# Kernel optimization log

Measured on AMD Instinct MI355X. Metric: run time of the kernel, lower is better.

Reference implementation:

```python
import jax, jax.numpy as jnp
import numpy as np

T = 4096        # sequence length
D = 128         # input feature dim
TRACE = 64      # trace_size
CONTEXT = 64    # context_size
HID = 64        # internal dense width (hardcoded 64 in module)
OUT = 128       # output_size
LN_EPS = 1e-6   # flax LayerNorm default epsilon


def setup_inputs() -> dict:
    key = jax.random.key(0)
    ks = jax.random.split(key, 12)

    def dense(k, fi, fo):
        return (jax.random.normal(k, (fi, fo), jnp.float32) / np.sqrt(fi).astype(np.float32))

    inp = {}
    inp["x"] = jax.random.normal(ks[0], (T, D), jnp.float32)
    inp["state"] = jnp.zeros((1, TRACE, CONTEXT), jnp.complex64)
    inp["start"] = jax.random.uniform(ks[1], (T,)) < 0.01  # sparse episode resets
    # deterministic FFM decay / frequency params (init_deterministic)
    inp["a"] = jnp.linspace(1e-6, 0.5, TRACE).astype(jnp.float32)
    inp["b"] = (2.0 * jnp.pi / jnp.linspace(1.0, 1000.0, CONTEXT)).astype(jnp.float32)
    inp["W1"] = dense(ks[2], D, HID);               inp["b1"] = jnp.zeros((HID,), jnp.float32)
    inp["W2"] = dense(ks[3], HID, 2 * TRACE);       inp["b2"] = jnp.zeros((2 * TRACE,), jnp.float32)
    inp["Wgi"] = dense(ks[4], 2 * TRACE, TRACE);    inp["bgi"] = jnp.zeros((TRACE,), jnp.float32)
    inp["Wp"] = dense(ks[5], 2 * TRACE, TRACE);     inp["bp"] = jnp.zeros((TRACE,), jnp.float32)
    inp["Wz"] = dense(ks[6], 2 * TRACE * CONTEXT, HID); inp["bz"] = jnp.zeros((HID,), jnp.float32)
    inp["Wgo"] = dense(ks[7], 2 * TRACE, HID);      inp["bgo"] = jnp.zeros((HID,), jnp.float32)
    inp["Ws"] = dense(ks[8], 2 * TRACE, HID);       inp["bs"] = jnp.zeros((HID,), jnp.float32)
    inp["W3"] = dense(ks[9], HID, HID);             inp["b3"] = jnp.zeros((HID,), jnp.float32)
    inp["W4"] = dense(ks[10], HID, OUT);            inp["b4"] = jnp.zeros((OUT,), jnp.float32)
    return inp


def _ffm_scan(scan_in, state0, start, a, b):
    # scan_in: (T, TRACE, CONTEXT) float, state0: (1, TRACE, CONTEXT) complex64
    t = scan_in.shape[0]
    timestep = jnp.ones((t + 1, 1, 1), dtype=jnp.int32)
    start_f = jnp.concatenate(
        [jnp.zeros((1, 1, 1), dtype=bool), start.reshape(t, 1, 1)], axis=0)
    xs = jnp.concatenate([state0, scan_in.astype(jnp.complex64)], axis=0)

    neg_a = -jnp.abs(a).reshape(1, TRACE, 1)
    b_r = b.reshape(1, 1, CONTEXT)
    ab = neg_a + 1j * b_r  # (1, TRACE, CONTEXT) complex

    def gamma(j):
        # j: (N,1,1) int -> (N, TRACE, CONTEXT) complex decay
        return jnp.exp(ab * j.astype(jnp.float32))

    def combine(carry, incoming):
        prev_start, s, i = carry
        st, xx, j = incoming
        keep = jnp.logical_not(st)
        s = s * keep
        j = j * keep.astype(j.dtype)
        new_s = s * gamma(j) + xx
        return (jnp.logical_or(st, prev_start), new_s, j + i)

    _, new_state, _ = jax.lax.associative_scan(
        combine, (start_f, xs, timestep), axis=0)
    return new_state[1:]  # (T, TRACE, CONTEXT) complex64


def _layernorm(x):
    mu = jnp.mean(x, axis=-1, keepdims=True)
    var = jnp.var(x, axis=-1, keepdims=True)
    return (x - mu) * jax.lax.rsqrt(var + LN_EPS)


def _forward(x, state, start, a, b, W1, b1, W2, b2, Wgi, bgi, Wp, bp,
             Wz, bz, Wgo, bgo, Ws, bs, W3, b3, W4, b4):
    h = jax.nn.relu(x @ W1 + b1)                 # (T, 64)
    h2 = h @ W2 + b2                             # (T, 2*TRACE)
    gate_in = jax.nn.sigmoid(h2 @ Wgi + bgi)     # (T, TRACE)
    pre = jax.nn.sigmoid(h2 @ Wp + bp)           # (T, TRACE)
    gated = pre * gate_in                        # (T, TRACE)
    scan_in = jnp.broadcast_to(gated[:, :, None], (gated.shape[0], TRACE, CONTEXT))
    state_seq = _ffm_scan(scan_in, state, start, a, b)  # (T, TRACE, CONTEXT) c64
    z_in = jnp.concatenate([jnp.real(state_seq), jnp.imag(state_seq)],
                           axis=-1).reshape(state_seq.shape[0], -1)
    z = z_in @ Wz + bz                           # (T, 64)
    gate_out = jax.nn.sigmoid(h2 @ Wgo + bgo)    # (T, 64)
    skip = h2 @ Ws + bs                          # (T, 64)
    out = _layernorm(z * gate_out) + skip * (1.0 - gate_out)
    out = jax.nn.relu(out @ W3 + b3)
    out = out @ W4 + b4                          # (T, OUT)
    return out, state_seq[-1:]


def reference(x, state, start, a, b, W1, b1, W2, b2, Wgi, bgi, Wp, bp,
              Wz, bz, Wgo, bgo, Ws, bs, W3, b3, W4, b4):
    return _forward(x, state, start, a, b, W1, b1, W2, b2, Wgi, bgi, Wp, bp,
                    Wz, bz, Wgo, bgo, Ws, bs, W3, b3, W4, b4)
```

## Files before the change

### kernel.cpp

```cpp
#include <hip/hip_runtime.h>
#include <math.h>

#define T_LEN 4096
#define D_IN 128
#define KDIM 4096
#define K2   8192

#define OFF_GATED 0u
#define OFF_GO    262144u
#define OFF_SKIP  524288u
#define OFF_PART  786432u
#define OFF_FLAGS 4980736u
#define OFF_CHS   4984832u
#define OFF_WZT   4984896u
#define OFF_SCR   5247040u

typedef __attribute__((ext_vector_type(8))) short short8v;
typedef __attribute__((ext_vector_type(4))) float float4v;

__device__ __forceinline__ float sigm(float x){ return 1.f/(1.f+expf(-x)); }
__device__ __forceinline__ unsigned short f2bf(float x){
    unsigned int u = __float_as_uint(x);
    return (unsigned short)((u + 0x7FFFu + ((u >> 16) & 1u)) >> 16);
}
__device__ __forceinline__ float wsum(float v) {
#pragma unroll
    for (int o = 32; o; o >>= 1) v += __shfl_xor(v, o, 64);
    return v;
}

__global__ __launch_bounds__(512) void k_prep(
    const unsigned char* __restrict__ su8, const int* __restrict__ si32,
    int* __restrict__ flags, int* __restrict__ chunkStart,
    const float* __restrict__ Wz, unsigned short* __restrict__ wzt,
    const float* __restrict__ x,
    const float* __restrict__ W1, const float* __restrict__ b1,
    const float* __restrict__ W2, const float* __restrict__ b2,
    const float* __restrict__ Wgi, const float* __restrict__ bgi,
    const float* __restrict__ Wp,  const float* __restrict__ bp,
    const float* __restrict__ Wgo, const float* __restrict__ bgo,
    const float* __restrict__ Wsk, const float* __restrict__ bsk,
    float* __restrict__ gated, float* __restrict__ go, float* __restrict__ sk)
{
    const int bx = blockIdx.x;
    const int tid = threadIdx.x;

    if (bx == 0) {
        __shared__ int cnt;
        if (tid == 0) cnt = 0;
        __syncthreads();
        int local = 0;
        for (int i = tid; i < 4096; i += 512)
            if (i & 3) local += su8[i];
        if (local) atomicAdd(&cnt, local);
        __syncthreads();
        if (cnt > 0) { for (int i = tid; i < 4096; i += 512) flags[i] = su8[i] ? 1 : 0; }
        else         { for (int i = tid; i < 4096; i += 512) flags[i] = si32[i] ? 1 : 0; }
        __syncthreads();
        if (tid < 64) {
            int any = 0;
#pragma unroll 8
            for (int j = 0; j < 64; ++j) any |= flags[tid * 64 + j];
            chunkStart[tid] = any;
        }
        return;
    }
    if (bx <= 64) {
        int idx = ((bx - 1) * 512 + tid) * 16;
        int j = idx >> 13, k0 = idx & 8191;
#pragma unroll
        for (int e = 0; e < 16; ++e) {
            int k = k0 + e;
            wzt[(size_t)j * K2 + k] = f2bf(Wz[(size_t)k * 64 + j]);
        }
        return;
    }

    __shared__ float xs[8][128];
    __shared__ float hs[8][64];
    __shared__ float h2s[8][128];
    __shared__ float tmp[8][4][64];
    const int t0 = (bx - 65) * 8;

    if (tid < 256) {
        int r = tid >> 5, kq = (tid & 31) << 2;
        *(float4*)&xs[r][kq] = *(const float4*)&x[(size_t)(t0 + r) * D_IN + kq];
    }

    const int j1 = tid >> 3, ks1 = tid & 7;
    float wr1[16];
#pragma unroll
    for (int kk = 0; kk < 16; ++kk) wr1[kk] = W1[(size_t)(ks1 * 16 + kk) * 64 + j1];
    const float bias1 = b1[j1];
    __syncthreads();
#pragma unroll
    for (int r = 0; r < 8; ++r) {
        float p = 0.f;
#pragma unroll
        for (int kq = 0; kq < 4; ++kq) {
            float4 xv = *(const float4*)&xs[r][ks1 * 16 + kq * 4];
            p += xv.x*wr1[kq*4] + xv.y*wr1[kq*4+1] + xv.z*wr1[kq*4+2] + xv.w*wr1[kq*4+3];
        }
        p += __shfl_xor(p, 1, 64); p += __shfl_xor(p, 2, 64); p += __shfl_xor(p, 4, 64);
        if (ks1 == 0) hs[r][j1] = fmaxf(p + bias1, 0.f);
    }
    __syncthreads();

    const int j2 = tid >> 2, ks2 = tid & 3;
    float wr2[16];
#pragma unroll
    for (int kk = 0; kk < 16; ++kk) wr2[kk] = W2[(size_t)(ks2 * 16 + kk) * 128 + j2];
    const float bias2 = b2[j2];
#pragma unroll
    for (int r = 0; r < 8; ++r) {
        float p = 0.f;
#pragma unroll
        for (int kq = 0; kq < 4; ++kq) {
            float4 hv = *(const float4*)&hs[r][ks2 * 16 + kq * 4];
            p += hv.x*wr2[kq*4] + hv.y*wr2[kq*4+1] + hv.z*wr2[kq*4+2] + hv.w*wr2[kq*4+3];
        }
        p += __shfl_xor(p, 1, 64); p += __shfl_xor(p, 2, 64);
        if (ks2 == 0) h2s[r][j2] = p + bias2;
    }
    __syncthreads();

    const int mat = tid >> 7, jj = (tid & 127) >> 1, kh = tid & 1;
    const float* Wm = (mat == 0) ? Wgi : (mat == 1) ? Wp : (mat == 2) ? Wgo : Wsk;
    float wgr[64];
#pragma unroll
    for (int kk = 0; kk < 64; ++kk) wgr[kk] = Wm[(size_t)(kh * 64 + kk) * 64 + jj];
#pragma unroll
    for (int r = 0; r < 8; ++r) {
        float p = 0.f;
#pragma unroll
        for (int kq = 0; kq < 16; ++kq) {
            float4 hv = *(const float4*)&h2s[r][kh * 64 + kq * 4];
            p += hv.x*wgr[kq*4] + hv.y*wgr[kq*4+1] + hv.z*wgr[kq*4+2] + hv.w*wgr[kq*4+3];
        }
        p += __shfl_xor(p, 1, 64);
        if (kh == 0) tmp[r][mat][jj] = p;
    }
    __syncthreads();

    {
        int r = tid >> 6, j = tid & 63;
        int t = t0 + r;
        float gi = sigm(tmp[r][0][j] + bgi[j]);
        float pr = sigm(tmp[r][1][j] + bp[j]);
        float g  = sigm(tmp[r][2][j] + bgo[j]);
        float s  = tmp[r][3][j] + bsk[j];
        gated[t * 64 + j] = gi * pr;
        go[t * 64 + j]    = g;
        sk[t * 64 + j]    = s;
    }
}

__global__ __launch_bounds__(512) void k_scanA(
    const float* __restrict__ gated, const int* __restrict__ flags,
    const float* __restrict__ a, const float* __restrict__ b,
    float2* __restrict__ carryB)
{
    const int p = threadIdx.x >> 6, c = threadIdx.x & 63;
    const int pair = blockIdx.x * 8 + p;
    const int ch = pair & 63, m = pair >> 6;
    const int t0 = ch * 64;

    const double ead = exp(-fabs((double)a[m]));
    const double bbd = (double)b[c];
    const float lre = (float)(ead * cos(bbd)), lim = (float)(ead * sin(bbd));
    float gv = gated[(size_t)(t0 + c) * 64 + m];
    unsigned long long fmask = __ballot(flags[t0 + c] != 0);
    float sre = 0.f, sim = 0.f;
#pragma unroll 8
    for (int j = 0; j < 64; ++j) {
        float g = __shfl(gv, j, 64);
        if ((fmask >> j) & 1) { sre = g; sim = 0.f; }
        else {
            float nr = fmaf(sre, lre, fmaf(-sim, lim, g));
            float ni = fmaf(sre, lim, sim * lre);
            sre = nr; sim = ni;
        }
    }
    carryB[(size_t)ch * KDIM + m * 64 + c] = make_float2(sre, sim);
}

__global__ __launch_bounds__(256) void k_scanBZ2(
    const float* __restrict__ gated, const int* __restrict__ flags,
    const int* __restrict__ chs,
    const float* __restrict__ a, const float* __restrict__ b,
    const float* __restrict__ st0,
    const float2* __restrict__ carryB,
    const unsigned short* __restrict__ wzt,
    float* __restrict__ part,
    float* __restrict__ out)
{
    const int tid = threadIdx.x;
    const int ml = tid >> 6, c = tid & 63;
    const int chpair = blockIdx.x & 31, mg = blockIdx.x >> 5;
    const int ch0 = chpair * 2;
    const int m = mg * 4 + ml;
    __shared__ unsigned short st[64 * 512];

    const float2* cbase = carryB + m * 64 + c;
    float2 BA[16], BB[16];
#define LOADB(dst, base)                                          \
    _Pragma("unroll")                                             \
    for (int q = 0; q < 16; ++q)                                  \
        dst[q] = cbase[(size_t)((base) + q) * KDIM];
    if (ch0 > 0)  { LOADB(BA, 0) }
    if (ch0 > 16) { LOADB(BB, 16) }

    float cre = st0[(m * 64 + c) * 2];
    float cim = st0[(m * 64 + c) * 2 + 1];
    unsigned long long cmask = __ballot(chs[c] != 0);

    const double ead = exp(-fabs((double)a[m]));
    const double bbd = (double)b[c];
    const float lre = (float)(ead * cos(bbd)), lim = (float)(ead * sin(bbd));
    const double ea64 = exp(-64.0 * fabs((double)a[m]));
    const float l64re = (float)(ea64 * cos(64.0 * bbd));
    const float l64im = (float)(ea64 * sin(64.0 * bbd));

#define COMB(src, base)                                           \
    _Pragma("unroll")                                             \
    for (int q = 0; q < 16; ++q) {                                \
        int chp = (base) + q;                                     \
        if (chp < ch0) {          \
            if ((cmask >> chp) & 1) { cre = src[q].x; cim = src[q].y; } \
            else {                                                \
                float nr = fmaf(cre, l64re, fmaf(-cim, l64im, src[q].x)); \
                float ni = fmaf(cre, l64im, fmaf(cim, l64re, src[q].y)); \
                cre = nr; cim = ni;                               \
            }                                                     \
        }                                                         \
    }
    if (ch0 > 0)  { COMB(BA, 0) }
    if (ch0 > 32) { LOADB(BA, 32) }
    if (ch0 > 16) { COMB(BB, 16) }
    if (ch0 > 48) { LOADB(BB, 48) }
    if (ch0 > 32) { COMB(BA, 32) }
    if (ch0 > 48) { COMB(BB, 48) }
#undef LOADB
#undef COMB

    const int l = c;
    const int jrow = ml * 16 + (l & 15);
    short8v bfr[16];
#pragma unroll
    for (int ks = 0; ks < 16; ++ks)
        bfr[ks] = *(const short8v*)&wzt[(size_t)jrow * K2 + mg * 512 + (ks * 4 + (l >> 4)) * 8];

    const int e0 = ml * 128 + c, e1 = e0 + 64;
    const int jcol = ml * 16 + (l & 15);

    for (int u = 0; u < 2; ++u) {
        const int ch = ch0 + u, t0s = ch * 64;

        float gv = gated[(size_t)(t0s + c) * 64 + m];
        unsigned long long fmask = __ballot(flags[t0s + c] != 0);
#pragma unroll 4
        for (int j = 0; j < 64; ++j) {
            float g = __shfl(gv, j, 64);
            if ((fmask >> j) & 1) { cre = g; cim = 0.f; }
            else {
                float nr = fmaf(cre, lre, fmaf(-cim, lim, g));
                float ni = fmaf(cre, lim, cim * lre);
                cre = nr; cim = ni;
            }
            const int sx = (j & 7) << 3;
            st[j * 512 + (e0 ^ sx)] = f2bf(cre);
            st[j * 512 + (e1 ^ sx)] = f2bf(cim);
        }
        if (ch == 63) {
            out[524288 + m * 64 + c]        = cre;
            out[524288 + 4096 + m * 64 + c] = cim;
        }
        __syncthreads();

        float4v acc[4];
#pragma unroll
        for (int i = 0; i < 4; ++i) acc[i] = (float4v){0.f, 0.f, 0.f, 0.f};
#pragma unroll
        for (int ks = 0; ks < 16; ++ks) {
#pragma unroll
            for (int mt = 0; mt < 4; ++mt) {
                const int row = mt * 16 + (l & 15);
                const int rchunk = (ks * 4 + (l >> 4)) ^ (row & 7);
                short8v af = *(const short8v*)&st[row * 512 + rchunk * 8];
                acc[mt] = __builtin_amdgcn_mfma_f32_16x16x32_bf16(af, bfr[ks], acc[mt], 0, 0, 0);
            }
        }

        float* pp = part + (size_t)mg * 262144;
#pragma unroll
        for (int mt = 0; mt < 4; ++mt) {
            const int trow = t0s + mt * 16 + (l >> 4) * 4;
#pragma unroll
            for (int r = 0; r < 4; ++r)
                pp[(size_t)(trow + r) * 64 + jcol] = acc[mt][r];
        }
        __syncthreads();
    }
}

__global__ __launch_bounds__(256) void k_epi(
    const float* __restrict__ part, const float* __restrict__ bz,
    const float* __restrict__ go, const float* __restrict__ sk,
    const float* __restrict__ W3, const float* __restrict__ b3,
    const float* __restrict__ W4, const float* __restrict__ b4,
    float* __restrict__ out)
{
    __shared__ float ob[16][64], hb[16][64];
    const int tid = threadIdx.x;
    const int w = tid >> 6, j = tid & 63;
    const int tbase = blockIdx.x * 16;

    const int j3 = tid >> 2, ks3 = tid & 3;
    float wgr3[16];
#pragma unroll
    for (int kk = 0; kk < 16; ++kk) wgr3[kk] = W3[(size_t)(ks3 * 16 + kk) * 64 + j3];
    const float b3v = b3[j3];
    const int j4 = tid >> 1, kh = tid & 1;
    float wgr4[32];
#pragma unroll
    for (int kk = 0; kk < 32; ++kk) wgr4[kk] = W4[(size_t)(kh * 32 + kk) * 128 + j4];
    const float b4v = b4[j4];

#pragma unroll
    for (int it = 0; it < 4; ++it) {
        const int r = it * 4 + w;
        const int t = tbase + r;
        float z = bz[j];
#pragma unroll
        for (int p = 0; p < 16; ++p) z += part[(size_t)p * 262144 + t * 64 + j];
        float g = go[t * 64 + j];
        float y = z * g;
        float mu = wsum(y) * 0.015625f;
        float d = y - mu;
        float var = wsum(d * d) * 0.015625f;
        ob[r][j] = d * (1.f / sqrtf(var + 1e-6f)) + sk[t * 64 + j] * (1.f - g);
    }
    __syncthreads();

#pragma unroll
    for (int r = 0; r < 16; ++r) {
        float p = 0.f;
#pragma unroll
        for (int kq = 0; kq < 4; ++kq) {
            float4 v = *(const float4*)&ob[r][ks3 * 16 + kq * 4];
            p += v.x*wgr3[kq*4] + v.y*wgr3[kq*4+1] + v.z*wgr3[kq*4+2] + v.w*wgr3[kq*4+3];
        }
        p += __shfl_xor(p, 1, 64); p += __shfl_xor(p, 2, 64);
        if (ks3 == 0) hb[r][j3] = fmaxf(p + b3v, 0.f);
    }
    __syncthreads();

#pragma unroll
    for (int r = 0; r < 16; ++r) {
        float p = 0.f;
#pragma unroll
        for (int kq = 0; kq < 8; ++kq) {
            float4 v = *(const float4*)&hb[r][kh * 32 + kq * 4];
            p += v.x*wgr4[kq*4] + v.y*wgr4[kq*4+1] + v.z*wgr4[kq*4+2] + v.w*wgr4[kq*4+3];
        }
        p += __shfl_xor(p, 1, 64);
        if (kh == 0) out[(size_t)(tbase + r) * 128 + j4] = p + b4v;
    }
}

extern "C" void kernel_launch(void* const* d_in, const int* in_sizes, int n_in,
                              void* d_out, int out_size, void* d_ws, size_t ws_size,
                              hipStream_t stream)
{
    const float* x   = (const float*)d_in[0];
    const float* st0 = (const float*)d_in[1];
    const void*  start = d_in[2];
    const float* a  = (const float*)d_in[3];
    const float* b  = (const float*)d_in[4];
    const float* W1 = (const float*)d_in[5];  const float* b1 = (const float*)d_in[6];
    const float* W2 = (const float*)d_in[7];  const float* b2 = (const float*)d_in[8];
    const float* Wgi= (const float*)d_in[9];  const float* bgi= (const float*)d_in[10];
    const float* Wp = (const float*)d_in[11]; const float* bp = (const float*)d_in[12];
    const float* Wz = (const float*)d_in[13]; const float* bz = (const float*)d_in[14];
    const float* Wgo= (const float*)d_in[15]; const float* bgo= (const float*)d_in[16];
    const float* Wsk= (const float*)d_in[17]; const float* bsk= (const float*)d_in[18];
    const float* W3 = (const float*)d_in[19]; const float* b3 = (const float*)d_in[20];
    const float* W4 = (const float*)d_in[21]; const float* b4 = (const float*)d_in[22];

    float* ws    = (float*)d_ws;
    float* out   = (float*)d_out;
    float* gated = ws + OFF_GATED;
    float* go    = ws + OFF_GO;
    float* sk    = ws + OFF_SKIP;
    float* part  = ws + OFF_PART;
    int*   flags = (int*)(ws + OFF_FLAGS);
    int*   chs   = (int*)(ws + OFF_CHS);
    unsigned short* wzt = (unsigned short*)(ws + OFF_WZT);
    float2* carryB = (float2*)(ws + OFF_SCR);

    hipLaunchKernelGGL(k_prep, dim3(577), dim3(512), 0, stream,
                       (const unsigned char*)start, (const int*)start, flags, chs,
                       Wz, wzt, x, W1, b1, W2, b2, Wgi, bgi, Wp, bp,
                       Wgo, bgo, Wsk, bsk, gated, go, sk);
    hipLaunchKernelGGL(k_scanA, dim3(512), dim3(512), 0, stream,
                       gated, flags, a, b, carryB);
    hipLaunchKernelGGL(k_scanBZ2, dim3(512), dim3(256), 0, stream,
                       gated, flags, chs, a, b, st0, carryB, wzt, part, out);
    hipLaunchKernelGGL(k_epi, dim3(256), dim3(256), 0, stream,
                       part, bz, go, sk, W3, b3, W4, b4, out);
}
```

Before: 78.07 us.

## Fuse chunk scan, Z projection and epilogue into one per-chunk kernel

```diff
diff --git a/kernel.cpp b/kernel.cpp
--- a/kernel.cpp
+++ b/kernel.cpp
@@ -9,11 +9,12 @@
 #define OFF_GATED 0u
 #define OFF_GO    262144u
 #define OFF_SKIP  524288u
-#define OFF_PART  786432u
+#define OFF_LAM   786432u
 #define OFF_FLAGS 4980736u
 #define OFF_CHS   4984832u
 #define OFF_WZT   4984896u
 #define OFF_SCR   5247040u
+#define OFF_CIN   5771328u
 
 typedef __attribute__((ext_vector_type(8))) short short8v;
 typedef __attribute__((ext_vector_type(4))) float float4v;
@@ -158,7 +159,7 @@
 __global__ __launch_bounds__(512) void k_scanA(
     const float* __restrict__ gated, const int* __restrict__ flags,
     const float* __restrict__ a, const float* __restrict__ b,
-    float2* __restrict__ carryB)
+    float2* __restrict__ carryB, float2* __restrict__ lam)
 {
     const int p = threadIdx.x >> 6, c = threadIdx.x & 63;
     const int pair = blockIdx.x * 8 + p;
@@ -168,12 +169,13 @@
     const double ead = exp(-fabs((double)a[m]));
     const double bbd = (double)b[c];
     const float lre = (float)(ead * cos(bbd)), lim = (float)(ead * sin(bbd));
-    float gv = gated[(size_t)(t0 + c) * 64 + m];
+    if (ch == 0) lam[m * 64 + c] = make_float2(lre, lim);
     unsigned long long fmask = __ballot(flags[t0 + c] != 0);
+    const float* grow = gated + (size_t)t0 * 64 + m;
     float sre = 0.f, sim = 0.f;
 #pragma unroll 8
     for (int j = 0; j < 64; ++j) {
-        float g = __shfl(gv, j, 64);
+        float g = grow[j * 64];
         if ((fmask >> j) & 1) { sre = g; sim = 0.f; }
         else {
             float nr = fmaf(sre, lre, fmaf(-sim, lim, g));
@@ -184,83 +186,112 @@
     carryB[(size_t)ch * KDIM + m * 64 + c] = make_float2(sre, sim);
 }
 
-__global__ __launch_bounds__(256) void k_scanBZ2(
+__global__ __launch_bounds__(256, 1) void k_scanZepi(
     const float* __restrict__ gated, const int* __restrict__ flags,
     const int* __restrict__ chs,
-    const float* __restrict__ a, const float* __restrict__ b,
-    const float* __restrict__ st0,
+    const float* __restrict__ st0, const float2* __restrict__ lam,
     const float2* __restrict__ carryB,
     const unsigned short* __restrict__ wzt,
-    float* __restrict__ part,
+    const float* __restrict__ go, const float* __restrict__ sk,
+    const float* __restrict__ bz,
+    const float* __restrict__ W3, const float* __restrict__ b3,
+    const float* __restrict__ W4, const float* __restrict__ b4,
+    float* __restrict__ cinW,
     float* __restrict__ out)
 {
     const int tid = threadIdx.x;
-    const int ml = tid >> 6, c = tid & 63;
-    const int chpair = blockIdx.x & 31, mg = blockIdx.x >> 5;
-    const int ch0 = chpair * 2;
-    const int m = mg * 4 + ml;
-    __shared__ unsigned short st[64 * 512];
-
-    const float2* cbase = carryB + m * 64 + c;
-    float2 BA[16], BB[16];
-#define LOADB(dst, base)                                          \
-    _Pragma("unroll")                                             \
-    for (int q = 0; q < 16; ++q)                                  \
-        dst[q] = cbase[(size_t)((base) + q) * KDIM];
-    if (ch0 > 0)  { LOADB(BA, 0) }
-    if (ch0 > 16) { LOADB(BB, 16) }
-
-    float cre = st0[(m * 64 + c) * 2];
-    float cim = st0[(m * 64 + c) * 2 + 1];
+    const int ml = tid >> 6, c = tid & 63, l = c;
+    const int ch = blockIdx.x, t0 = ch * 64;
+    __shared__ __align__(16) char smem[65536];
+    unsigned short* st = (unsigned short*)smem;
+
     unsigned long long cmask = __ballot(chs[c] != 0);
-
-    const double ead = exp(-fabs((double)a[m]));
-    const double bbd = (double)b[c];
-    const float lre = (float)(ead * cos(bbd)), lim = (float)(ead * sin(bbd));
-    const double ea64 = exp(-64.0 * fabs((double)a[m]));
-    const float l64re = (float)(ea64 * cos(64.0 * bbd));
-    const float l64im = (float)(ea64 * sin(64.0 * bbd));
-
-#define COMB(src, base)                                           \
-    _Pragma("unroll")                                             \
-    for (int q = 0; q < 16; ++q) {                                \
-        int chp = (base) + q;                                     \
-        if (chp < ch0) {          \
-            if ((cmask >> chp) & 1) { cre = src[q].x; cim = src[q].y; } \
-            else {                                                \
-                float nr = fmaf(cre, l64re, fmaf(-cim, l64im, src[q].x)); \
-                float ni = fmaf(cre, l64im, fmaf(cim, l64re, src[q].y)); \
-                cre = nr; cim = ni;                               \
-            }                                                     \
-        }                                                         \
-    }
-    if (ch0 > 0)  { COMB(BA, 0) }
-    if (ch0 > 32) { LOADB(BA, 32) }
-    if (ch0 > 16) { COMB(BB, 16) }
-    if (ch0 > 48) { LOADB(BB, 48) }
-    if (ch0 > 32) { COMB(BA, 32) }
-    if (ch0 > 48) { COMB(BB, 48) }
-#undef LOADB
-#undef COMB
-
-    const int l = c;
-    const int jrow = ml * 16 + (l & 15);
-    short8v bfr[16];
-#pragma unroll
-    for (int ks = 0; ks < 16; ++ks)
-        bfr[ks] = *(const short8v*)&wzt[(size_t)jrow * K2 + mg * 512 + (ks * 4 + (l >> 4)) * 8];
-
+    unsigned long long fmask = __ballot(flags[t0 + c] != 0);
+
+    float cinr[16], cini[16], l64r[16], l64i[16];
+#pragma unroll
+    for (int mg = 0; mg < 16; ++mg) {
+        int mm = mg * 4 + ml;
+        float2 lv = lam[mm * 64 + c];
+        float ar = lv.x, ai = lv.y;
+#pragma unroll
+        for (int s = 0; s < 6; ++s) { float nr = ar*ar - ai*ai; float ni = 2.f*ar*ai; ar = nr; ai = ni; }
+        l64r[mg] = ar; l64i[mg] = ai;
+        cinr[mg] = st0[(mm * 64 + c) * 2];
+        cini[mg] = st0[(mm * 64 + c) * 2 + 1];
+    }
+
+    {
+        float2 A0[16], A1[16];
+        int chp = 0;
+        for (; chp + 1 < ch; chp += 2) {
+#pragma unroll
+            for (int mg = 0; mg < 16; ++mg) A0[mg] = carryB[(size_t)chp * KDIM + (mg*4+ml)*64 + c];
+#pragma unroll
+            for (int mg = 0; mg < 16; ++mg) A1[mg] = carryB[(size_t)(chp+1) * KDIM + (mg*4+ml)*64 + c];
+            const bool s0 = (cmask >> chp) & 1;
+            const bool s1 = (cmask >> (chp + 1)) & 1;
+#pragma unroll
+            for (int mg = 0; mg < 16; ++mg) {
+                if (s0) { cinr[mg] = A0[mg].x; cini[mg] = A0[mg].y; }
+                else {
+                    float nr = fmaf(cinr[mg], l64r[mg], fmaf(-cini[mg], l64i[mg], A0[mg].x));
+                    float ni = fmaf(cinr[mg], l64i[mg], fmaf(cini[mg], l64r[mg], A0[mg].y));
+                    cinr[mg] = nr; cini[mg] = ni;
+                }
+            }
+#pragma unroll
+            for (int mg = 0; mg < 16; ++mg) {
+                if (s1) { cinr[mg] = A1[mg].x; cini[mg] = A1[mg].y; }
+                else {
+                    float nr = fmaf(cinr[mg], l64r[mg], fmaf(-cini[mg], l64i[mg], A1[mg].x));
+                    float ni = fmaf(cinr[mg], l64i[mg], fmaf(cini[mg], l64r[mg], A1[mg].y));
+                    cinr[mg] = nr; cini[mg] = ni;
+                }
+            }
+        }
+        if (chp < ch) {
+#pragma unroll
+            for (int mg = 0; mg < 16; ++mg) A0[mg] = carryB[(size_t)chp * KDIM + (mg*4+ml)*64 + c];
+            const bool s0 = (cmask >> chp) & 1;
+#pragma unroll
+            for (int mg = 0; mg < 16; ++mg) {
+                if (s0) { cinr[mg] = A0[mg].x; cini[mg] = A0[mg].y; }
+                else {
+                    float nr = fmaf(cinr[mg], l64r[mg], fmaf(-cini[mg], l64i[mg], A0[mg].x));
+                    float ni = fmaf(cinr[mg], l64i[mg], fmaf(cini[mg], l64r[mg], A0[mg].y));
+                    cinr[mg] = nr; cini[mg] = ni;
+                }
+            }
+        }
+    }
+
+    float* cb = cinW + (size_t)ch * 8192;
+#pragma unroll
+    for (int mg = 0; mg < 16; ++mg) {
+        cb[(mg * 2 + 0) * 256 + ml * 64 + c] = cinr[mg];
+        cb[(mg * 2 + 1) * 256 + ml * 64 + c] = cini[mg];
+    }
+
+    float4v acc[4];
+#pragma unroll
+    for (int i = 0; i < 4; ++i) acc[i] = (float4v){0.f, 0.f, 0.f, 0.f};
     const int e0 = ml * 128 + c, e1 = e0 + 64;
-    const int jcol = ml * 16 + (l & 15);
-
-    for (int u = 0; u < 2; ++u) {
-        const int ch = ch0 + u, t0s = ch * 64;
-
-        float gv = gated[(size_t)(t0s + c) * 64 + m];
-        unsigned long long fmask = __ballot(flags[t0s + c] != 0);
+#pragma unroll 1
+    for (int mg = 0; mg < 16; ++mg) {
+        const int mm = mg * 4 + ml;
+        float2 lv = lam[mm * 64 + c];
+        const float lre = lv.x, lim = lv.y;
+        short8v bfr[16];
+#pragma unroll
+        for (int ks = 0; ks < 16; ++ks)
+            bfr[ks] = *(const short8v*)&wzt[(size_t)(ml*16 + (l&15)) * K2 + mg*512 + (ks*4 + (l>>4))*8];
+        float cre = cb[(mg * 2 + 0) * 256 + ml * 64 + c];
+        float cim = cb[(mg * 2 + 1) * 256 + ml * 64 + c];
+        const float* grow = gated + (size_t)t0 * 64 + mm;
 #pragma unroll 4
         for (int j = 0; j < 64; ++j) {
-            float g = __shfl(gv, j, 64);
+            float g = grow[j * 64];
             if ((fmask >> j) & 1) { cre = g; cim = 0.f; }
             else {
                 float nr = fmaf(cre, lre, fmaf(-cim, lim, g));
@@ -272,16 +303,12 @@
             st[j * 512 + (e1 ^ sx)] = f2bf(cim);
         }
         if (ch == 63) {
-            out[524288 + m * 64 + c]        = cre;
-            out[524288 + 4096 + m * 64 + c] = cim;
+            out[524288 + mm * 64 + c]        = cre;
+            out[524288 + 4096 + mm * 64 + c] = cim;
         }
         __syncthreads();
-
-        float4v acc[4];
-#pragma unroll
-        for (int i = 0; i < 4; ++i) acc[i] = (float4v){0.f, 0.f, 0.f, 0.f};
-#pragma unroll
-        for (int ks = 0; ks < 16; ++ks) {
+#pragma unroll
+        for (int ks = 0; ks < 16; ++ks)
 #pragma unroll
             for (int mt = 0; mt < 4; ++mt) {
                 const int row = mt * 16 + (l & 15);
@@ -289,31 +316,8 @@
                 short8v af = *(const short8v*)&st[row * 512 + rchunk * 8];
                 acc[mt] = __builtin_amdgcn_mfma_f32_16x16x32_bf16(af, bfr[ks], acc[mt], 0, 0, 0);
             }
-        }
-
-        float* pp = part + (size_t)mg * 262144;
-#pragma unroll
-        for (int mt = 0; mt < 4; ++mt) {
-            const int trow = t0s + mt * 16 + (l >> 4) * 4;
-#pragma unroll
-            for (int r = 0; r < 4; ++r)
-                pp[(size_t)(trow + r) * 64 + jcol] = acc[mt][r];
-        }
         __syncthreads();
     }
-}
-
-__global__ __launch_bounds__(256) void k_epi(
-    const float* __restrict__ part, const float* __restrict__ bz,
-    const float* __restrict__ go, const float* __restrict__ sk,
-    const float* __restrict__ W3, const float* __restrict__ b3,
-    const float* __restrict__ W4, const float* __restrict__ b4,
-    float* __restrict__ out)
-{
-    __shared__ float ob[16][64], hb[16][64];
-    const int tid = threadIdx.x;
-    const int w = tid >> 6, j = tid & 63;
-    const int tbase = blockIdx.x * 16;
 
     const int j3 = tid >> 2, ks3 = tid & 3;
     float wgr3[16];
@@ -326,24 +330,33 @@
     for (int kk = 0; kk < 32; ++kk) wgr4[kk] = W4[(size_t)(kh * 32 + kk) * 128 + j4];
     const float b4v = b4[j4];
 
-#pragma unroll
-    for (int it = 0; it < 4; ++it) {
-        const int r = it * 4 + w;
-        const int t = tbase + r;
-        float z = bz[j];
-#pragma unroll
-        for (int p = 0; p < 16; ++p) z += part[(size_t)p * 262144 + t * 64 + j];
-        float g = go[t * 64 + j];
+    float (*zb)[64] = (float(*)[64])smem;
+    float (*ob)[64] = (float(*)[64])(smem + 16384);
+    float (*hb)[64] = (float(*)[64])(smem + 32768);
+    const int jcol = ml * 16 + (l & 15);
+#pragma unroll
+    for (int mt = 0; mt < 4; ++mt) {
+        const int tr = mt * 16 + (l >> 4) * 4;
+#pragma unroll
+        for (int r = 0; r < 4; ++r) zb[tr + r][jcol] = acc[mt][r];
+    }
+    __syncthreads();
+
+#pragma unroll
+    for (int it = 0; it < 16; ++it) {
+        const int r = it * 4 + ml, t = t0 + r;
+        float z = zb[r][c] + bz[c];
+        float g = go[t * 64 + c];
         float y = z * g;
         float mu = wsum(y) * 0.015625f;
         float d = y - mu;
         float var = wsum(d * d) * 0.015625f;
-        ob[r][j] = d * (1.f / sqrtf(var + 1e-6f)) + sk[t * 64 + j] * (1.f - g);
-    }
-    __syncthreads();
-
-#pragma unroll
-    for (int r = 0; r < 16; ++r) {
+        ob[r][c] = d * (1.f / sqrtf(var + 1e-6f)) + sk[t * 64 + c] * (1.f - g);
+    }
+    __syncthreads();
+
+#pragma unroll 4
+    for (int r = 0; r < 64; ++r) {
         float p = 0.f;
 #pragma unroll
         for (int kq = 0; kq < 4; ++kq) {
@@ -355,8 +368,8 @@
     }
     __syncthreads();
 
-#pragma unroll
-    for (int r = 0; r < 16; ++r) {
+#pragma unroll 4
+    for (int r = 0; r < 64; ++r) {
         float p = 0.f;
 #pragma unroll
         for (int kq = 0; kq < 8; ++kq) {
@@ -364,7 +377,7 @@
             p += v.x*wgr4[kq*4] + v.y*wgr4[kq*4+1] + v.z*wgr4[kq*4+2] + v.w*wgr4[kq*4+3];
         }
         p += __shfl_xor(p, 1, 64);
-        if (kh == 0) out[(size_t)(tbase + r) * 128 + j4] = p + b4v;
+        if (kh == 0) out[(size_t)(t0 + r) * 128 + j4] = p + b4v;
     }
 }
 
@@ -392,20 +405,20 @@
     float* gated = ws + OFF_GATED;
     float* go    = ws + OFF_GO;
     float* sk    = ws + OFF_SKIP;
-    float* part  = ws + OFF_PART;
     int*   flags = (int*)(ws + OFF_FLAGS);
     int*   chs   = (int*)(ws + OFF_CHS);
     unsigned short* wzt = (unsigned short*)(ws + OFF_WZT);
     float2* carryB = (float2*)(ws + OFF_SCR);
+    float2* lam    = (float2*)(ws + OFF_LAM);
+    float*  cinW   = ws + OFF_CIN;
 
     hipLaunchKernelGGL(k_prep, dim3(577), dim3(512), 0, stream,
                        (const unsigned char*)start, (const int*)start, flags, chs,
                        Wz, wzt, x, W1, b1, W2, b2, Wgi, bgi, Wp, bp,
                        Wgo, bgo, Wsk, bsk, gated, go, sk);
     hipLaunchKernelGGL(k_scanA, dim3(512), dim3(512), 0, stream,
-                       gated, flags, a, b, carryB);
-    hipLaunchKernelGGL(k_scanBZ2, dim3(512), dim3(256), 0, stream,
-                       gated, flags, chs, a, b, st0, carryB, wzt, part, out);
-    hipLaunchKernelGGL(k_epi, dim3(256), dim3(256), 0, stream,
-                       part, bz, go, sk, W3, b3, W4, b4, out);
-}
+                       gated, flags, a, b, carryB, lam);
+    hipLaunchKernelGGL(k_scanZepi, dim3(64), dim3(256), 0, stream,
+                       gated, flags, chs, st0, (const float2*)lam, (const float2*)carryB,
+                       wzt, go, sk, bz, W3, b3, W4, b4, cinW, out);
+}
```

After: 217.8 us. +178.9%, slower.
